# Performance work log

Measured on AMD Instinct MI355X. Metric: run time of the kernel, lower is better.

The kernel has to match this reference:

```python
import jax, jax.numpy as jnp
import numpy as np

N = 128          # system size (8*8*2), hard-coded in SpectrumLoss
M_LANCZOS = 10   # Lanczos(m=10)
KAPPA = 0.276


def dd_opt(x, U1, kappa):
    # Wilson-style 2D hopping operator (stand-in for the external DDOpt).
    # x: (B,8,8,2) fields, U1: (B,8,8,2) real gauge links (2 directions).
    u0 = U1[..., 0:1]
    u1 = U1[..., 1:2]
    hop = (u0 * jnp.roll(x, -1, axis=1)
           + u1 * jnp.roll(x, -1, axis=2)
           + jnp.roll(u0 * x, 1, axis=1)
           + jnp.roll(u1 * x, 1, axis=2))
    return x - kappa * hop


def build_lower_tri(net_out):
    # Row-major packing of a lower-triangular NxN matrix (torch.tril_indices order).
    B = net_out.shape[0]
    r, c = jnp.tril_indices(N)
    L = jnp.zeros((B, N, N), net_out.dtype)
    return L.at[:, r, c].set(net_out)


def matvect(L, U1, x):
    # x: (B, N). Preconditioned operator: L (L^T (D x)).
    B = x.shape[0]
    y = dd_opt(x.reshape(B, 8, 8, 2), U1, KAPPA).reshape(B, N)
    y = jnp.einsum('bij,bi->bj', L, y)  # upper_tri_mat: M^H v (real -> M^T v)
    y = jnp.einsum('bij,bj->bi', L, y)  # lower_tri_matvect: L v
    return y


def lanczos(Av, v0):
    # Standard batched Lanczos producing symmetric tridiagonal T (B, M, M).
    B = v0.shape[0]

    def step(carry, _):
        v_prev, v_cur, beta = carry
        w = Av(v_cur)
        alpha = jnp.sum(w * v_cur, axis=1)
        w = w - alpha[:, None] * v_cur - beta[:, None] * v_prev
        beta_new = jnp.linalg.norm(w, axis=1)
        v_next = w / (beta_new[:, None] + 1e-30)
        return (v_cur, v_next, beta_new), (alpha, beta_new)

    init = (jnp.zeros_like(v0), v0, jnp.zeros((B,), v0.dtype))
    _, (alphas, betas) = jax.lax.scan(step, init, None, length=M_LANCZOS)
    alphas = alphas.T  # (B, M)
    betas = betas.T    # (B, M); last beta unused
    T = jnp.zeros((B, M_LANCZOS, M_LANCZOS), v0.dtype)
    i = jnp.arange(M_LANCZOS)
    T = T.at[:, i, i].set(alphas)
    j = jnp.arange(M_LANCZOS - 1)
    T = T.at[:, j, j + 1].set(betas[:, :-1])
    T = T.at[:, j + 1, j].set(betas[:, :-1])
    return T


def setup_inputs() -> dict:
    key = jax.random.key(0)
    k1, k2, k3 = jax.random.split(key, 3)
    B = 2048
    net_out = jax.random.normal(k1, (B, N * (N + 1) // 2), dtype=jnp.float32)
    U1 = jax.random.uniform(k2, (B, 8, 8, 2), dtype=jnp.float32)
    v = jax.random.normal(k3, (B, N), dtype=jnp.float32)
    return {"net_out": net_out, "U1": U1, "v": v}


def reference(net_out, U1, v):
    vn = v / jnp.linalg.norm(v, axis=1, keepdims=True)
    L = build_lower_tri(net_out)
    T = lanczos(lambda x: matvect(L, U1, x), vn)
    eig = jnp.abs(jnp.linalg.eigvalsh(T))  # symmetric tridiagonal -> real eigvals
    max_e = jnp.max(eig, axis=1)
    min_e = jnp.min(eig, axis=1)
    return jnp.mean(max_e ** 2) - jnp.mean(min_e ** 2)
```

## Files before the change

### kernel.cpp

```cpp
#include <hip/hip_runtime.h>
#include <hip/hip_bf16.h>
#include <math.h>

#define NN 128
#define TRI 8256
#define BATCH 2048
#define M_L 10
#define KAPPA 0.276f

using half8  = __attribute__((ext_vector_type(8))) _Float16;
using half2v = __attribute__((ext_vector_type(2))) _Float16;
using f32x4  = __attribute__((ext_vector_type(4))) float;

static __device__ inline float dot2h(unsigned m, unsigned y, float c) {
#if __has_builtin(__builtin_amdgcn_fdot2)
    return __builtin_amdgcn_fdot2(__builtin_bit_cast(half2v, m),
                                  __builtin_bit_cast(half2v, y), c, false);
#else
    half2v a = __builtin_bit_cast(half2v, m), b = __builtin_bit_cast(half2v, y);
    return c + (float)a.x * (float)b.x + (float)a.y * (float)b.y;
#endif
}

__device__ inline int sturm_count10(const double* a, const double* off2, double x) {
    double pm = 1.0;
    double p  = a[0] - x;
    int c = (p < 0.0);
    #pragma unroll
    for (int i = 1; i < M_L; i++) {
        double pn = (a[i] - x) * p - off2[i - 1] * pm;
        c += ((pn < 0.0) != (p < 0.0));
        pm = p; p = pn;
    }
    return c;
}

__global__ __launch_bounds__(256, 5) void lanczos_kernel(
    const float* __restrict__ net_out,
    const float* __restrict__ U1,
    const float* __restrict__ v_in,
    float* __restrict__ contrib)
{
    __shared__ __align__(16) _Float16 Msh[128 * 128];
    unsigned* ys  = (unsigned*)Msh;
    float*    part = (float*)(Msh + 128);
    float*    ab_s = (float*)(Msh + 640);

    const int b = blockIdx.x;
    const int t = threadIdx.x;
    const int lane = t & 63;
    const int w = t >> 6;

    float2 vv = {0.f, 0.f}, uu = {0.f, 0.f};
    if (w == 0) {
        vv = *(const float2*)(v_in + (size_t)b * NN + 2 * lane);
        uu = *(const float2*)(U1 + (size_t)b * 128 + 2 * lane);
    }

    {
        unsigned long long* z = (unsigned long long*)Msh;
        #pragma unroll
        for (int k = t; k < 128 * 128 / 4; k += 256) z[k] = 0ULL;
    }
    __syncthreads();

    {
        const float4* src4 = (const float4*)(net_out + (size_t)b * TRI);
        for (int q = t; q < TRI / 4; q += 256) {
            float4 f = src4[q];
            const int e = 4 * q;
            float vals[4] = {f.x, f.y, f.z, f.w};
            #pragma unroll
            for (int i = 0; i < 4; i++) {
                int ei = e + i;
                int r = (int)((sqrtf((float)(8 * ei) + 1.0f) - 1.0f) * 0.5f);
                int c = ei - ((r * (r + 1)) >> 1);
                Msh[r * 128 + (c ^ ((r & 7) << 3))] = (_Float16)vals[i];
            }
        }
    }
    __syncthreads();

    {
        const int m = lane & 15;
        const int g = lane >> 4;
        const int sw = (m & 7) << 3;
        f32x4 acc[2][8];
        #pragma unroll
        for (int bi = 0; bi < 2; bi++)
            #pragma unroll
            for (int j = 0; j < 8; j++) acc[bi][j] = (f32x4){0.f, 0.f, 0.f, 0.f};
        const int band0 = w, band1 = w + 4;
        #pragma unroll
        for (int kc = 0; kc < 4; kc++) {
            const int col = (kc * 32 + g * 8) ^ sw;
            half8 a0 = *(const half8*)&Msh[(16 * band0 + m) * 128 + col];
            half8 a1 = *(const half8*)&Msh[(16 * band1 + m) * 128 + col];
            #pragma unroll
            for (int j = 0; j < 8; j++) {
                half8 bfr = *(const half8*)&Msh[(16 * j + m) * 128 + col];
                acc[0][j] = __builtin_amdgcn_mfma_f32_16x16x32_f16(a0, bfr, acc[0][j], 0, 0, 0);
                acc[1][j] = __builtin_amdgcn_mfma_f32_16x16x32_f16(a1, bfr, acc[1][j], 0, 0, 0);
            }
        }
        __syncthreads();

        #pragma unroll
        for (int bi = 0; bi < 2; bi++) {
            const int band = (bi == 0) ? band0 : band1;
            #pragma unroll
            for (int j = 0; j < 8; j++) {
                f32x4 a = acc[bi][j];
                half2v p01 = {(_Float16)a[0], (_Float16)a[1]};
                half2v p23 = {(_Float16)a[2], (_Float16)a[3]};
                uint2 pk;
                pk.x = __builtin_bit_cast(unsigned, p01);
                pk.y = __builtin_bit_cast(unsigned, p23);
                const int colw = (16 * band + 4 * g) ^ sw;
                *(uint2*)&Msh[(16 * j + m) * 128 + colw] = pk;
            }
        }
    }
    __syncthreads();

    const int r = t & 127, h = t >> 7;
    uint4 Mr[8];
    {
        const int rsw = r & 7;
        #pragma unroll
        for (int k = 0; k < 8; k++)
            Mr[k] = *(const uint4*)&Msh[r * 128 + ((64 * h) | ((k ^ rsw) << 3))];
    }
    __syncthreads();

    float x0 = 0.f, x1 = 0.f, p0 = 0.f, p1 = 0.f, beta = 0.f;
    float u0c = 0.f, u1c = 0.f, u0m = 0.f, u1m = 0.f;
    const int l_ip = (lane + 8) & 63;
    const int l_jp = (lane & 56) | ((lane + 1) & 7);
    const int l_im = (lane + 56) & 63;
    const int l_jm = (lane & 56) | ((lane + 7) & 7);

    if (w == 0) {
        float s = vv.x * vv.x + vv.y * vv.y;
        #pragma unroll
        for (int o = 1; o < 64; o <<= 1) s += __shfl_xor(s, o, 64);
        float inv = 1.0f / sqrtf(s);
        x0 = vv.x * inv; x1 = vv.y * inv;
        u0c = uu.x; u1c = uu.y;
        u0m = __shfl(u0c, l_im, 64);
        u1m = __shfl(u1c, l_jm, 64);

        float a0 = __shfl(x0, l_ip, 64), a1 = __shfl(x1, l_ip, 64);
        float b0 = __shfl(x0, l_jp, 64), b1 = __shfl(x1, l_jp, 64);
        float c0 = __shfl(x0, l_im, 64), c1 = __shfl(x1, l_im, 64);
        float d0 = __shfl(x0, l_jm, 64), d1 = __shfl(x1, l_jm, 64);
        float y0 = x0 - KAPPA * (u0c * a0 + u1c * b0 + u0m * c0 + u1m * d0);
        float y1 = x1 - KAPPA * (u0c * a1 + u1c * b1 + u0m * c1 + u1m * d1);
        half2v yp = {(_Float16)y0, (_Float16)y1};
        ys[lane] = __builtin_bit_cast(unsigned, yp);
    }
    __syncthreads();

    const uint4* Y4 = (const uint4*)&ys[32 * h];

    for (int it = 0; it < M_L; it++) {
        {
            float aA = 0.f, aB = 0.f, aC = 0.f, aD = 0.f;
            #pragma unroll
            for (int c = 0; c < 8; c += 4) {
                uint4 y_0 = Y4[c],     y_1 = Y4[c + 1];
                uint4 y_2 = Y4[c + 2], y_3 = Y4[c + 3];
                aA = dot2h(Mr[c].x,     y_0.x, aA); aA = dot2h(Mr[c].y,     y_0.y, aA);
                aA = dot2h(Mr[c].z,     y_0.z, aA); aA = dot2h(Mr[c].w,     y_0.w, aA);
                aB = dot2h(Mr[c + 1].x, y_1.x, aB); aB = dot2h(Mr[c + 1].y, y_1.y, aB);
                aB = dot2h(Mr[c + 1].z, y_1.z, aB); aB = dot2h(Mr[c + 1].w, y_1.w, aB);
                aC = dot2h(Mr[c + 2].x, y_2.x, aC); aC = dot2h(Mr[c + 2].y, y_2.y, aC);
                aC = dot2h(Mr[c + 2].z, y_2.z, aC); aC = dot2h(Mr[c + 2].w, y_2.w, aC);
                aD = dot2h(Mr[c + 3].x, y_3.x, aD); aD = dot2h(Mr[c + 3].y, y_3.y, aD);
                aD = dot2h(Mr[c + 3].z, y_3.z, aD); aD = dot2h(Mr[c + 3].w, y_3.w, aD);
            }
            part[t] = (aA + aB) + (aC + aD);
        }
        __syncthreads();

        if (w == 0) {
            float2 pa = *(const float2*)&part[2 * lane];
            float2 pb = *(const float2*)&part[128 + 2 * lane];
            float z0 = pa.x + pb.x;
            float z1 = pa.y + pb.y;

            float s1 = z0 * x0 + z1 * x1;
            float s2 = z0 * z0 + z1 * z1;
            float s3 = z0 * p0 + z1 * p1;
            #pragma unroll
            for (int o = 1; o < 64; o <<= 1) {
                s1 += __shfl_xor(s1, o, 64);
                s2 += __shfl_xor(s2, o, 64);
                s3 += __shfl_xor(s3, o, 64);
            }
            float alpha = s1;
            float b2 = s2 - alpha * alpha - beta * (2.0f * s3 - beta);
            float bn = sqrtf(fmaxf(b2, 0.0f));
            float w0 = z0 - alpha * x0 - beta * p0;
            float w1 = z1 - alpha * x1 - beta * p1;
            float inv = 1.0f / (bn + 1e-30f);
            p0 = x0; p1 = x1;
            x0 = w0 * inv; x1 = w1 * inv;
            beta = bn;
            if (lane == 0) {
                ab_s[it]      = alpha;
                ab_s[10 + it] = bn;
            }

            float a0 = __shfl(x0, l_ip, 64), a1 = __shfl(x1, l_ip, 64);
            float b0 = __shfl(x0, l_jp, 64), b1 = __shfl(x1, l_jp, 64);
            float c0 = __shfl(x0, l_im, 64), c1 = __shfl(x1, l_im, 64);
            float d0 = __shfl(x0, l_jm, 64), d1 = __shfl(x1, l_jm, 64);
            float y0 = x0 - KAPPA * (u0c * a0 + u1c * b0 + u0m * c0 + u1m * d0);
            float y1 = x1 - KAPPA * (u0c * a1 + u1c * b1 + u0m * c1 + u1m * d1);
            half2v yp = {(_Float16)y0, (_Float16)y1};
            ys[lane] = __builtin_bit_cast(unsigned, yp);
        }
        __syncthreads();
    }

    if (w != (b & 3)) return;

    double a[M_L], off2[M_L - 1], offa[M_L - 1];
    #pragma unroll
    for (int i = 0; i < M_L; i++) a[i] = (double)ab_s[i];
    #pragma unroll
    for (int i = 0; i < M_L - 1; i++) {
        double bb = (double)ab_s[10 + i];
        offa[i] = fabs(bb);
        off2[i] = bb * bb;
    }
    double glo = 1e300, ghi = -1e300;
    #pragma unroll
    for (int i = 0; i < M_L; i++) {
        double rr = 0.0;
        if (i > 0) rr += offa[i - 1];
        if (i < M_L - 1) rr += offa[i];
        glo = fmin(glo, a[i] - rr);
        ghi = fmax(ghi, a[i] + rr);
    }

    const int kk = lane & 31;
    const bool topHalf = (lane >= 32);

    const int K = topHalf ? 1 : M_L;
    double lo = glo, hi = ghi;
    for (int round = 0; round < 4; round++) {
        double wdt = (hi - lo) * (1.0 / 33.0);
        double x = lo + wdt * (double)(kk + 1);
        int cnt = sturm_count10(a, off2, x);
        unsigned long long m64 = __ballot(cnt >= K);
        unsigned mm = topHalf ? (unsigned)(m64 >> 32)
                              : (unsigned)(m64 & 0xffffffffu);
        int p = (mm == 0u) ? 32 : (__ffs(mm) - 1);
        double nlo = lo + wdt * (double)p;
        hi = (mm == 0u) ? hi : (lo + wdt * (double)(p + 1));
        lo = nlo;
    }
    double mid = 0.5 * (lo + hi);
    double lmax = __shfl(mid, 0, 64);
    double lmin = __shfl(mid, 32, 64);
    double maxabs = fmax(fabs(lmax), fabs(lmin));

    double wlo = 0.0, whi = maxabs;
    for (int round = 0; round < 4; round++) {
        double wdt = (whi - wlo) * (1.0 / 33.0);
        double s = wlo + wdt * (double)(kk + 1);
        double x = topHalf ? -s : s;
        int cnt = sturm_count10(a, off2, x);
        int o = __shfl_xor(cnt, 32, 64);
        int inwin = topHalf ? (o - cnt) : (cnt - o);
        unsigned long long m64 = __ballot(inwin >= 1);
        unsigned mm = (unsigned)(m64 & 0xffffffffu);
        int p = (mm == 0u) ? 32 : (__ffs(mm) - 1);
        double nlo = wlo + wdt * (double)p;
        whi = (mm == 0u) ? whi : (wlo + wdt * (double)(p + 1));
        wlo = nlo;
    }
    double minabs = 0.5 * (wlo + whi);
    if (lane == 0) contrib[b] = (float)(maxabs * maxabs - minabs * minabs);
}

__global__ __launch_bounds__(1024) void reduce_kernel(
    const float* __restrict__ contrib, float* __restrict__ out)
{
    __shared__ float red[16];
    int t = threadIdx.x;
    float s = contrib[t] + contrib[t + 1024];
    #pragma unroll
    for (int o = 32; o > 0; o >>= 1) s += __shfl_down(s, o, 64);
    if ((t & 63) == 0) red[t >> 6] = s;
    __syncthreads();
    if (t < 64) {
        float r = (t < 16) ? red[t] : 0.0f;
        #pragma unroll
        for (int o = 8; o > 0; o >>= 1) r += __shfl_down(r, o, 64);
        if (t == 0) out[0] = r / (float)BATCH;
    }
}

extern "C" void kernel_launch(void* const* d_in, const int* in_sizes, int n_in,
                              void* d_out, int out_size, void* d_ws, size_t ws_size,
                              hipStream_t stream) {
    const float* net_out = (const float*)d_in[0];
    const float* U1      = (const float*)d_in[1];
    const float* v       = (const float*)d_in[2];
    float* contrib = (float*)d_ws;

    lanczos_kernel<<<BATCH, 256, 0, stream>>>(net_out, U1, v, contrib);
    reduce_kernel<<<1, 1024, 0, stream>>>(contrib, (float*)d_out);
}
```

Baseline: 134.1 us.

## Keep Gram matrix in MFMA accumulators and do matvec from registers

Stops writing the MFMA-computed M = L·Lᵀ product back to shared memory as fp16 and reloading it per row. Each Lanczos matvec is now computed straight from the fp32 accumulator fragments held in registers, with a cross-lane shuffle reduction and per-wave partial sums combined by wave 0. The y vector is kept in fp32 instead of fp16, and the Sturm count now reads the tridiagonal coefficients from LDS instead of caching them in double registers. Together these cut register and LDS traffic and improve precision, but they add shuffles and a 4-way partial reduction to every iteration.

```diff
diff --git a/kernel.cpp b/kernel.cpp
--- a/kernel.cpp
+++ b/kernel.cpp
@@ -12,23 +12,14 @@
 using half2v = __attribute__((ext_vector_type(2))) _Float16;
 using f32x4  = __attribute__((ext_vector_type(4))) float;
 
-static __device__ inline float dot2h(unsigned m, unsigned y, float c) {
-#if __has_builtin(__builtin_amdgcn_fdot2)
-    return __builtin_amdgcn_fdot2(__builtin_bit_cast(half2v, m),
-                                  __builtin_bit_cast(half2v, y), c, false);
-#else
-    half2v a = __builtin_bit_cast(half2v, m), b = __builtin_bit_cast(half2v, y);
-    return c + (float)a.x * (float)b.x + (float)a.y * (float)b.y;
-#endif
-}
-
-__device__ inline int sturm_count10(const double* a, const double* off2, double x) {
+__device__ inline int sturm_lds(const float* __restrict__ ab_s, double x) {
     double pm = 1.0;
-    double p  = a[0] - x;
+    double p  = (double)ab_s[0] - x;
     int c = (p < 0.0);
     #pragma unroll
     for (int i = 1; i < M_L; i++) {
-        double pn = (a[i] - x) * p - off2[i - 1] * pm;
+        double bb = (double)ab_s[10 + i - 1];
+        double pn = ((double)ab_s[i] - x) * p - (bb * bb) * pm;
         c += ((pn < 0.0) != (p < 0.0));
         pm = p; p = pn;
     }
@@ -42,9 +33,9 @@
     float* __restrict__ contrib)
 {
     __shared__ __align__(16) _Float16 Msh[128 * 128];
-    unsigned* ys  = (unsigned*)Msh;
-    float*    part = (float*)(Msh + 128);
-    float*    ab_s = (float*)(Msh + 640);
+    float* ysf  = (float*)Msh;
+    float* part = (float*)(Msh + 256);
+    float* ab_s = (float*)(Msh + 1280);
 
     const int b = blockIdx.x;
     const int t = threadIdx.x;
@@ -81,11 +72,11 @@
     }
     __syncthreads();
 
+    const int m = lane & 15;
+    const int g = lane >> 4;
+    f32x4 acc[2][8];
     {
-        const int m = lane & 15;
-        const int g = lane >> 4;
         const int sw = (m & 7) << 3;
-        f32x4 acc[2][8];
         #pragma unroll
         for (int bi = 0; bi < 2; bi++)
             #pragma unroll
@@ -103,33 +94,6 @@
                 acc[1][j] = __builtin_amdgcn_mfma_f32_16x16x32_f16(a1, bfr, acc[1][j], 0, 0, 0);
             }
         }
-        __syncthreads();
-
-        #pragma unroll
-        for (int bi = 0; bi < 2; bi++) {
-            const int band = (bi == 0) ? band0 : band1;
-            #pragma unroll
-            for (int j = 0; j < 8; j++) {
-                f32x4 a = acc[bi][j];
-                half2v p01 = {(_Float16)a[0], (_Float16)a[1]};
-                half2v p23 = {(_Float16)a[2], (_Float16)a[3]};
-                uint2 pk;
-                pk.x = __builtin_bit_cast(unsigned, p01);
-                pk.y = __builtin_bit_cast(unsigned, p23);
-                const int colw = (16 * band + 4 * g) ^ sw;
-                *(uint2*)&Msh[(16 * j + m) * 128 + colw] = pk;
-            }
-        }
-    }
-    __syncthreads();
-
-    const int r = t & 127, h = t >> 7;
-    uint4 Mr[8];
-    {
-        const int rsw = r & 7;
-        #pragma unroll
-        for (int k = 0; k < 8; k++)
-            Mr[k] = *(const uint4*)&Msh[r * 128 + ((64 * h) | ((k ^ rsw) << 3))];
     }
     __syncthreads();
 
@@ -156,38 +120,38 @@
         float d0 = __shfl(x0, l_jm, 64), d1 = __shfl(x1, l_jm, 64);
         float y0 = x0 - KAPPA * (u0c * a0 + u1c * b0 + u0m * c0 + u1m * d0);
         float y1 = x1 - KAPPA * (u0c * a1 + u1c * b1 + u0m * c1 + u1m * d1);
-        half2v yp = {(_Float16)y0, (_Float16)y1};
-        ys[lane] = __builtin_bit_cast(unsigned, yp);
-    }
-    __syncthreads();
-
-    const uint4* Y4 = (const uint4*)&ys[32 * h];
+        *(float2*)&ysf[2 * lane] = (float2){y0, y1};
+    }
+    __syncthreads();
 
     for (int it = 0; it < M_L; it++) {
         {
-            float aA = 0.f, aB = 0.f, aC = 0.f, aD = 0.f;
-            #pragma unroll
-            for (int c = 0; c < 8; c += 4) {
-                uint4 y_0 = Y4[c],     y_1 = Y4[c + 1];
-                uint4 y_2 = Y4[c + 2], y_3 = Y4[c + 3];
-                aA = dot2h(Mr[c].x,     y_0.x, aA); aA = dot2h(Mr[c].y,     y_0.y, aA);
-                aA = dot2h(Mr[c].z,     y_0.z, aA); aA = dot2h(Mr[c].w,     y_0.w, aA);
-                aB = dot2h(Mr[c + 1].x, y_1.x, aB); aB = dot2h(Mr[c + 1].y, y_1.y, aB);
-                aB = dot2h(Mr[c + 1].z, y_1.z, aB); aB = dot2h(Mr[c + 1].w, y_1.w, aB);
-                aC = dot2h(Mr[c + 2].x, y_2.x, aC); aC = dot2h(Mr[c + 2].y, y_2.y, aC);
-                aC = dot2h(Mr[c + 2].z, y_2.z, aC); aC = dot2h(Mr[c + 2].w, y_2.w, aC);
-                aD = dot2h(Mr[c + 3].x, y_3.x, aD); aD = dot2h(Mr[c + 3].y, y_3.y, aD);
-                aD = dot2h(Mr[c + 3].z, y_3.z, aD); aD = dot2h(Mr[c + 3].w, y_3.w, aD);
-            }
-            part[t] = (aA + aB) + (aC + aD);
+            float4 yb0 = *(const float4*)&ysf[16 * w + 4 * g];
+            float4 yb1 = *(const float4*)&ysf[16 * (w + 4) + 4 * g];
+            float z[8];
+            #pragma unroll
+            for (int j = 0; j < 8; j++) {
+                f32x4 A0 = acc[0][j], A1 = acc[1][j];
+                float zj = A0[0] * yb0.x + A0[1] * yb0.y + A0[2] * yb0.z + A0[3] * yb0.w
+                         + A1[0] * yb1.x + A1[1] * yb1.y + A1[2] * yb1.z + A1[3] * yb1.w;
+                zj += __shfl_xor(zj, 16, 64);
+                zj += __shfl_xor(zj, 32, 64);
+                z[j] = zj;
+            }
+            if (lane < 16) {
+                #pragma unroll
+                for (int j = 0; j < 8; j++) part[w * 128 + 16 * j + lane] = z[j];
+            }
         }
         __syncthreads();
 
         if (w == 0) {
-            float2 pa = *(const float2*)&part[2 * lane];
-            float2 pb = *(const float2*)&part[128 + 2 * lane];
-            float z0 = pa.x + pb.x;
-            float z1 = pa.y + pb.y;
+            float z0 = 0.f, z1 = 0.f;
+            #pragma unroll
+            for (int ww = 0; ww < 4; ww++) {
+                float2 pw = *(const float2*)&part[ww * 128 + 2 * lane];
+                z0 += pw.x; z1 += pw.y;
+            }
 
             float s1 = z0 * x0 + z1 * x1;
             float s2 = z0 * z0 + z1 * z1;
@@ -218,31 +182,22 @@
             float d0 = __shfl(x0, l_jm, 64), d1 = __shfl(x1, l_jm, 64);
             float y0 = x0 - KAPPA * (u0c * a0 + u1c * b0 + u0m * c0 + u1m * d0);
             float y1 = x1 - KAPPA * (u0c * a1 + u1c * b1 + u0m * c1 + u1m * d1);
-            half2v yp = {(_Float16)y0, (_Float16)y1};
-            ys[lane] = __builtin_bit_cast(unsigned, yp);
+            *(float2*)&ysf[2 * lane] = (float2){y0, y1};
         }
         __syncthreads();
     }
 
     if (w != (b & 3)) return;
 
-    double a[M_L], off2[M_L - 1], offa[M_L - 1];
-    #pragma unroll
-    for (int i = 0; i < M_L; i++) a[i] = (double)ab_s[i];
-    #pragma unroll
-    for (int i = 0; i < M_L - 1; i++) {
-        double bb = (double)ab_s[10 + i];
-        offa[i] = fabs(bb);
-        off2[i] = bb * bb;
-    }
     double glo = 1e300, ghi = -1e300;
     #pragma unroll
     for (int i = 0; i < M_L; i++) {
+        double ai = (double)ab_s[i];
         double rr = 0.0;
-        if (i > 0) rr += offa[i - 1];
-        if (i < M_L - 1) rr += offa[i];
-        glo = fmin(glo, a[i] - rr);
-        ghi = fmax(ghi, a[i] + rr);
+        if (i > 0)        rr += fabs((double)ab_s[10 + i - 1]);
+        if (i < M_L - 1)  rr += fabs((double)ab_s[10 + i]);
+        glo = fmin(glo, ai - rr);
+        ghi = fmax(ghi, ai + rr);
     }
 
     const int kk = lane & 31;
@@ -253,7 +208,7 @@
     for (int round = 0; round < 4; round++) {
         double wdt = (hi - lo) * (1.0 / 33.0);
         double x = lo + wdt * (double)(kk + 1);
-        int cnt = sturm_count10(a, off2, x);
+        int cnt = sturm_lds(ab_s, x);
         unsigned long long m64 = __ballot(cnt >= K);
         unsigned mm = topHalf ? (unsigned)(m64 >> 32)
                               : (unsigned)(m64 & 0xffffffffu);
@@ -272,7 +227,7 @@
         double wdt = (whi - wlo) * (1.0 / 33.0);
         double s = wlo + wdt * (double)(kk + 1);
         double x = topHalf ? -s : s;
-        int cnt = sturm_count10(a, off2, x);
+        int cnt = sturm_lds(ab_s, x);
         int o = __shfl_xor(cnt, 32, 64);
         int inwin = topHalf ? (o - cnt) : (cnt - o);
         unsigned long long m64 = __ballot(inwin >= 1);
```

Measured after the change: 162.8 us. 1.21x slower.
